# Optimization experiments

Measured on AMD Instinct MI355X. Metric: run time of the kernel, lower is better.

## Reference

```python
import jax, jax.numpy as jnp
import numpy as np

N = 100000
IN_CH, HID_CH, OUT_CH = 128, 128, 64
E = 1600000


def gcn_layer(x, W, b, src, dst, num_nodes):
    """PyG GCNConv: add self-loops, symmetric deg^-1/2 normalization,
    x' = D^-1/2 (A+I) D^-1/2 (x W) + b."""
    # degrees including self-loops (deg = 1 + in-degree with unit edge weights)
    ones = jnp.ones(dst.shape[0], dtype=x.dtype)
    deg = jnp.ones(num_nodes, dtype=x.dtype).at[dst].add(ones)
    dinv = jax.lax.rsqrt(deg)
    h = x @ W  # [N, out_dim] -- transform before propagate (PyG order)
    # neighbor messages
    norm = dinv[src] * dinv[dst]                      # [E]
    msg = h[src] * norm[:, None]                      # [E, out_dim] (traffic-bound)
    agg = jax.ops.segment_sum(msg, dst, num_segments=num_nodes)
    # self-loop contribution: norm_ii = dinv[i]^2
    agg = agg + h * (dinv * dinv)[:, None]
    return agg + b


def setup_inputs() -> dict:
    key = jax.random.key(0)
    ks = jax.random.split(key, 7)
    x = jax.random.normal(ks[0], (N, IN_CH), dtype=jnp.float32)
    edge_index = jax.random.randint(ks[1], (2, E), 0, N, dtype=jnp.int64)
    # Glorot-style init like PyG GCNConv
    W1 = jax.random.normal(ks[2], (IN_CH, HID_CH), dtype=jnp.float32) * (1.0 / np.sqrt(IN_CH))
    b1 = jnp.zeros((HID_CH,), dtype=jnp.float32)
    W2 = jax.random.normal(ks[3], (HID_CH, OUT_CH), dtype=jnp.float32) * (1.0 / np.sqrt(HID_CH))
    b2 = jnp.zeros((OUT_CH,), dtype=jnp.float32)
    return {"x": x, "edge_index": edge_index, "W1": W1, "b1": b1, "W2": W2, "b2": b2}


def reference(x, edge_index, W1, b1, W2, b2):
    src, dst = edge_index[0], edge_index[1]
    h = gcn_layer(x, W1, b1, src, dst, N)
    h = jax.nn.relu(h)  # dropout is identity in eval mode
    out = gcn_layer(h, W2, b2, src, dst, N)
    return out
```

## Files before the change

### kernel.cpp

```cpp
#include <hip/hip_runtime.h>
#include <hip/hip_fp16.h>

#define NNODES 100000
#define NEDGES 1600000
#define IN_C   128
#define HID_C  128
#define OUT_C  64

#define CAP     64
#define OVF_MAX 4096

#define BUCKET_SHIFT 7
#define BUCKET_NODES 128
#define NB ((NNODES + BUCKET_NODES - 1) / BUCKET_NODES)
#define BCAP 3072
#define EB 4096
#define NBLK_A ((NEDGES + EB - 1) / EB)

typedef __attribute__((ext_vector_type(8))) _Float16 half8;
typedef __attribute__((ext_vector_type(4))) _Float16 half4;
typedef __attribute__((ext_vector_type(4))) float floatx4;

__device__ __forceinline__ long long load_idx(const void* p, long long i, int is64) {
  return is64 ? ((const long long*)p)[i] : (long long)((const int*)p)[i];
}

__global__ void detect_idx_kernel(const void* eidx, int* flag) {
  const unsigned* w = (const unsigned*)eidx;
  int lane = threadIdx.x & 63;
  unsigned v = w[2 * lane + 1];
  unsigned long long bad = __ballot(v != 0u);
  if (lane == 0) *flag = (bad == 0ull) ? 1 : 0;
}


__global__ void zero_misc_kernel(int* bcnt, int* ovf_cnt, int* ovfA_cnt) {
  int i = blockIdx.x * 256 + threadIdx.x;
  if (i < NB) bcnt[i] = 0;
  if (i == 0) { *ovf_cnt = 0; *ovfA_cnt = 0; }
}

__global__ __launch_bounds__(256) void binA_kernel(const void* __restrict__ eidx,
                                                   const int* __restrict__ flag,
                                                   int* __restrict__ bcnt,
                                                   unsigned* __restrict__ buf,
                                                   int* __restrict__ ovfA_cnt,
                                                   int2* __restrict__ ovfA) {
  __shared__ int hist[NB];
  __shared__ int base[NB];
  __shared__ int ofs[NB];
  const int tid = threadIdx.x;
  const int e0 = blockIdx.x * EB;
  const int e1 = min(e0 + EB, NEDGES);
  const int is64 = *flag;

  for (int b = tid; b < NB; b += 256) { hist[b] = 0; ofs[b] = 0; }
  __syncthreads();

  for (int e = e0 + tid; e < e1; e += 256) {
    int d = (int)load_idx(eidx, (long long)NEDGES + e, is64);
    atomicAdd(&hist[d >> BUCKET_SHIFT], 1);
  }
  __syncthreads();

  for (int b = tid; b < NB; b += 256) {
    int h = hist[b];
    if (h > 0) base[b] = atomicAdd(&bcnt[b], h);
  }
  __syncthreads();

  for (int e = e0 + tid; e < e1; e += 256) {
    int s = (int)load_idx(eidx, e, is64);
    int d = (int)load_idx(eidx, (long long)NEDGES + e, is64);
    int b = d >> BUCKET_SHIFT;
    int ko = atomicAdd(&ofs[b], 1);
    int slot = base[b] + ko;
    if (slot < BCAP) {
      buf[(size_t)b * BCAP + slot] =
          (unsigned)s | ((unsigned)(d & (BUCKET_NODES - 1)) << 17);
    } else {
      int p = atomicAdd(ovfA_cnt, 1);
      if (p < OVF_MAX) ovfA[p] = make_int2(s, d);
    }
  }
}

__global__ __launch_bounds__(256) void binB_kernel(const int* __restrict__ bcnt,
                                                   const unsigned* __restrict__ buf,
                                                   int* __restrict__ cnt,
                                                   float* __restrict__ dinv,
                                                   int* __restrict__ pad_csr,
                                                   int* __restrict__ ovf_cnt,
                                                   int2* __restrict__ ovf) {
  __shared__ int pad[BUCKET_NODES * CAP];
  __shared__ int lcnt[BUCKET_NODES];
  const int b = blockIdx.x;
  const int tid = threadIdx.x;
  const int node0 = b << BUCKET_SHIFT;

  if (tid < BUCKET_NODES) lcnt[tid] = 0;
  __syncthreads();

  const int n = min(bcnt[b], BCAP);
  for (int k = tid; k < n; k += 256) {
    unsigned u = buf[(size_t)b * BCAP + k];
    int s = (int)(u & 0x1FFFFu);
    int dl = (int)(u >> 17);
    int slot = atomicAdd(&lcnt[dl], 1);
    if (slot < CAP) {
      pad[dl * CAP + slot] = s;
    } else {
      int p = atomicAdd(ovf_cnt, 1);
      if (p < OVF_MAX) ovf[p] = make_int2(s, node0 + dl);
    }
  }
  __syncthreads();

  constexpr int I4PN = CAP / 4;
  for (int q = tid; q < BUCKET_NODES * I4PN; q += 256) {
    int dl = q / I4PN;
    int gn = node0 + dl;
    if (gn < NNODES) {
      int c = (q % I4PN) * 4;
      *(int4*)&pad_csr[(size_t)gn * CAP + c] = *(const int4*)&pad[dl * CAP + c];
    }
  }
  if (tid < BUCKET_NODES && node0 + tid < NNODES) {
    int c = lcnt[tid];
    cnt[node0 + tid] = c;
    dinv[node0 + tid] = rsqrtf((float)(c + 1));
  }
}

__global__ void fixup_kernel(const int* __restrict__ ovfA_cnt,
                             const int2* __restrict__ ovfA,
                             int* __restrict__ cnt, float* __restrict__ dinv,
                             int* __restrict__ pad_csr,
                             int* __restrict__ ovf_cnt, int2* __restrict__ ovf) {
  int n = min(*ovfA_cnt, OVF_MAX);
  for (int t = threadIdx.x; t < n; t += 256) {
    int2 p = ovfA[t];
    int k = atomicAdd(&cnt[p.y], 1);
    if (k < CAP) {
      pad_csr[(size_t)p.y * CAP + k] = p.x;
    } else {
      int q = atomicAdd(ovf_cnt, 1);
      if (q < OVF_MAX) ovf[q] = p;
    }
  }
  __syncthreads();
  for (int t = threadIdx.x; t < n; t += 256) {
    int node = ovfA[t].y;
    dinv[node] = rsqrtf((float)(cnt[node] + 1));
  }
}

struct F8 {
  float x0, x1, x2, x3, x4, x5, x6, x7;
};

__device__ __forceinline__ void add_h8(F8& a, const __half* p) {
  int4 r = *(const int4*)p;
  const __half2* h = (const __half2*)&r;
  float2 f0 = __half22float2(h[0]);
  float2 f1 = __half22float2(h[1]);
  float2 f2 = __half22float2(h[2]);
  float2 f3 = __half22float2(h[3]);
  a.x0 += f0.x; a.x1 += f0.y; a.x2 += f1.x; a.x3 += f1.y;
  a.x4 += f2.x; a.x5 += f2.y; a.x6 += f3.x; a.x7 += f3.y;
}

template <int C, bool RELU, bool OUT16>
__global__ __launch_bounds__(256) void gather_kernel(const int* __restrict__ cnt,
                                                     const int* __restrict__ pad_csr,
                                                     const float* __restrict__ dinv,
                                                     const __half* __restrict__ Hs,
                                                     const float* __restrict__ bias,
                                                     const int* __restrict__ ovf_cnt,
                                                     const int2* __restrict__ ovf,
                                                     void* __restrict__ OutPtr) {
  constexpr int TPN = C / 8;
  int gid = blockIdx.x * 256 + threadIdx.x;
  int i = gid / TPN;
  int c8 = (gid % TPN) * 8;
  if (i >= NNODES) return;

  const float di = dinv[i];
  const int deg = cnt[i];
  const int beg = i * CAP;
  const int end = beg + min(deg, CAP);
  const int* __restrict__ lst = pad_csr;

  F8 a0 = {}, a1 = {}, a2 = {}, a3 = {};
  add_h8(a0, &Hs[(size_t)i * C + c8]);

  int j = beg;
  for (; j + 8 <= end; j += 8) {
    int4 sa = *(const int4*)&lst[j];
    int4 sb = *(const int4*)&lst[j + 4];
    add_h8(a0, &Hs[(size_t)sa.x * C + c8]);
    add_h8(a1, &Hs[(size_t)sa.y * C + c8]);
    add_h8(a2, &Hs[(size_t)sa.z * C + c8]);
    add_h8(a3, &Hs[(size_t)sa.w * C + c8]);
    add_h8(a0, &Hs[(size_t)sb.x * C + c8]);
    add_h8(a1, &Hs[(size_t)sb.y * C + c8]);
    add_h8(a2, &Hs[(size_t)sb.z * C + c8]);
    add_h8(a3, &Hs[(size_t)sb.w * C + c8]);
  }
  for (; j + 2 <= end; j += 2) {
    int s0 = lst[j + 0], s1 = lst[j + 1];
    add_h8(a0, &Hs[(size_t)s0 * C + c8]);
    add_h8(a1, &Hs[(size_t)s1 * C + c8]);
  }
  if (j < end) {
    add_h8(a0, &Hs[(size_t)lst[j] * C + c8]);
  }

  if (deg > CAP) {
    int n = min(*ovf_cnt, OVF_MAX);
    for (int t = 0; t < n; ++t) {
      int2 p = ovf[t];
      if (p.y == i) add_h8(a0, &Hs[(size_t)p.x * C + c8]);
    }
  }

  float s0 = a0.x0 + a1.x0 + a2.x0 + a3.x0;
  float s1 = a0.x1 + a1.x1 + a2.x1 + a3.x1;
  float s2 = a0.x2 + a1.x2 + a2.x2 + a3.x2;
  float s3 = a0.x3 + a1.x3 + a2.x3 + a3.x3;
  float s4 = a0.x4 + a1.x4 + a2.x4 + a3.x4;
  float s5 = a0.x5 + a1.x5 + a2.x5 + a3.x5;
  float s6 = a0.x6 + a1.x6 + a2.x6 + a3.x6;
  float s7 = a0.x7 + a1.x7 + a2.x7 + a3.x7;

  float4 b0 = *(const float4*)&bias[c8];
  float4 b1 = *(const float4*)&bias[c8 + 4];
  float o0 = fmaf(s0, di, b0.x);
  float o1 = fmaf(s1, di, b0.y);
  float o2 = fmaf(s2, di, b0.z);
  float o3 = fmaf(s3, di, b0.w);
  float o4 = fmaf(s4, di, b1.x);
  float o5 = fmaf(s5, di, b1.y);
  float o6 = fmaf(s6, di, b1.z);
  float o7 = fmaf(s7, di, b1.w);
  if (RELU) {
    o0 = o0 > 0.f ? o0 : 0.f;
    o1 = o1 > 0.f ? o1 : 0.f;
    o2 = o2 > 0.f ? o2 : 0.f;
    o3 = o3 > 0.f ? o3 : 0.f;
    o4 = o4 > 0.f ? o4 : 0.f;
    o5 = o5 > 0.f ? o5 : 0.f;
    o6 = o6 > 0.f ? o6 : 0.f;
    o7 = o7 > 0.f ? o7 : 0.f;
  }
  if (OUT16) {
    half8 hv = {(_Float16)o0, (_Float16)o1, (_Float16)o2, (_Float16)o3,
                (_Float16)o4, (_Float16)o5, (_Float16)o6, (_Float16)o7};
    *(half8*)((_Float16*)OutPtr + (size_t)i * C + c8) = hv;
  } else {
    float* Out = (float*)OutPtr;
    float4 v0 = make_float4(o0, o1, o2, o3);
    float4 v1 = make_float4(o4, o5, o6, o7);
    *(float4*)&Out[(size_t)i * C + c8] = v0;
    *(float4*)&Out[(size_t)i * C + c8 + 4] = v1;
  }
}

template <int K, int N, bool A_F16>
__global__ __launch_bounds__(256) void mfma_gemm_kernel(const void* __restrict__ Xv,
                                                        const float* __restrict__ Wm,
                                                        const float* __restrict__ scale,
                                                        _Float16* __restrict__ Hout,
                                                        int M) {
  constexpr int KP = K + 8;
  __shared__ alignas(16) _Float16 Alds[64 * KP];
  __shared__ alignas(16) _Float16 Wlds[N * KP];

  const int tid = threadIdx.x;
  const int row0 = blockIdx.x * 64;

  constexpr int TILES = (K / 4) * (N / 4);
  for (int tile = tid; tile < TILES; tile += 256) {
    int kt = tile / (N / 4);
    int nt = tile % (N / 4);
    const float* wp = &Wm[(4 * kt) * N + 4 * nt];
    float4 r0 = *(const float4*)(wp);
    float4 r1 = *(const float4*)(wp + N);
    float4 r2 = *(const float4*)(wp + 2 * N);
    float4 r3 = *(const float4*)(wp + 3 * N);
    half4 c0 = {(_Float16)r0.x, (_Float16)r1.x, (_Float16)r2.x, (_Float16)r3.x};
    half4 c1 = {(_Float16)r0.y, (_Float16)r1.y, (_Float16)r2.y, (_Float16)r3.y};
    half4 c2 = {(_Float16)r0.z, (_Float16)r1.z, (_Float16)r2.z, (_Float16)r3.z};
    half4 c3 = {(_Float16)r0.w, (_Float16)r1.w, (_Float16)r2.w, (_Float16)r3.w};
    *(half4*)&Wlds[(4 * nt + 0) * KP + 4 * kt] = c0;
    *(half4*)&Wlds[(4 * nt + 1) * KP + 4 * kt] = c1;
    *(half4*)&Wlds[(4 * nt + 2) * KP + 4 * kt] = c2;
    *(half4*)&Wlds[(4 * nt + 3) * KP + 4 * kt] = c3;
  }

  if (A_F16) {
    const _Float16* Xh = (const _Float16*)Xv;
    constexpr int H8PR = K / 8;
    constexpr int TOT = 64 * H8PR;
    for (int idx = tid; idx < TOT; idx += 256) {
      int lr = idx / H8PR;
      int c8 = (idx % H8PR) * 8;
      int gr = row0 + lr;
      if (gr > M - 1) gr = M - 1;
      int4 v = *(const int4*)&Xh[(size_t)gr * K + c8];
      *(int4*)&Alds[lr * KP + c8] = v;
    }
  } else {
    const float* Xf = (const float*)Xv;
    constexpr int F4PR = K / 4;
    constexpr int TOT = 64 * F4PR;
    for (int idx = tid; idx < TOT; idx += 256) {
      int lr = idx / F4PR;
      int c4 = (idx % F4PR) * 4;
      int gr = row0 + lr;
      if (gr > M - 1) gr = M - 1;
      float4 v = *(const float4*)&Xf[(size_t)gr * K + c4];
      half4 h = {(_Float16)v.x, (_Float16)v.y, (_Float16)v.z, (_Float16)v.w};
      *(half4*)&Alds[lr * KP + c4] = h;
    }
  }
  __syncthreads();

  const int w = tid >> 6;
  const int lane = tid & 63;
  const int g = lane >> 4;
  const int mi = lane & 15;
  constexpr int NT = N / 16;

  floatx4 acc[NT];
#pragma unroll
  for (int t = 0; t < NT; ++t) acc[t] = (floatx4){0.f, 0.f, 0.f, 0.f};

  const _Float16* arow = &Alds[(w * 16 + mi) * KP];
#pragma unroll
  for (int ks = 0; ks < K / 32; ++ks) {
    half8 a = *(const half8*)(arow + ks * 32 + g * 8);
#pragma unroll
    for (int t = 0; t < NT; ++t) {
      half8 b = *(const half8*)&Wlds[(t * 16 + mi) * KP + ks * 32 + g * 8];
      acc[t] = __builtin_amdgcn_mfma_f32_16x16x32_f16(a, b, acc[t], 0, 0, 0);
    }
  }

#pragma unroll
  for (int r = 0; r < 4; ++r) {
    int grow = row0 + w * 16 + 4 * g + r;
    if (grow < M) {
      float s = scale[grow];
      _Float16* orow = Hout + (size_t)grow * N + mi;
#pragma unroll
      for (int t = 0; t < NT; ++t) orow[t * 16] = (_Float16)(acc[t][r] * s);
    }
  }
}

extern "C" void kernel_launch(void* const* d_in, const int* in_sizes, int n_in,
                              void* d_out, int out_size, void* d_ws, size_t ws_size,
                              hipStream_t stream) {
  const float* x = (const float*)d_in[0];
  const void* eidx = d_in[1];
  const float* W1 = (const float*)d_in[2];
  const float* b1 = (const float*)d_in[3];
  const float* W2 = (const float*)d_in[4];
  const float* b2 = (const float*)d_in[5];
  float* out = (float*)d_out;
  char* ws = (char*)d_ws;

  int*      flag     = (int*)(ws + 0);
  int*      ovf_cnt  = (int*)(ws + 512);
  int*      ovfA_cnt = (int*)(ws + 1024);
  int*      bcnt     = (int*)(ws + 1536);
  int*      cnt      = (int*)(ws + 8192);
  float*    dinv     = (float*)(ws + 408576);
  int2*     ovf      = (int2*)(ws + 809472);
  int2*     ovfA     = (int2*)(ws + 842752);
  unsigned* buf      = (unsigned*)(ws + 876032);
  int*      pad_csr  = (int*)(ws + 10486272);
  _Float16* h1       = (_Float16*)(ws + 36086784);
  _Float16* hidden   = (_Float16*)(ws + 61687296);
  _Float16* h2 = h1;

  detect_idx_kernel<<<1, 64, 0, stream>>>(eidx, flag);
  zero_misc_kernel<<<(NB + 255) / 256, 256, 0, stream>>>(bcnt, ovf_cnt, ovfA_cnt);
  binA_kernel<<<NBLK_A, 256, 0, stream>>>(eidx, flag, bcnt, buf, ovfA_cnt, ovfA);
  binB_kernel<<<NB, 256, 0, stream>>>(bcnt, buf, cnt, dinv, pad_csr, ovf_cnt, ovf);
  fixup_kernel<<<1, 256, 0, stream>>>(ovfA_cnt, ovfA, cnt, dinv, pad_csr,
                                      ovf_cnt, ovf);

  const int GB = (NNODES + 63) / 64;

  mfma_gemm_kernel<IN_C, HID_C, false>
      <<<GB, 256, 0, stream>>>(x, W1, dinv, h1, NNODES);
  gather_kernel<HID_C, true, true>
      <<<(NNODES * (HID_C / 8) + 255) / 256, 256, 0, stream>>>(cnt, pad_csr, dinv,
                                                               (const __half*)h1, b1,
                                                               ovf_cnt, ovf, hidden);
  mfma_gemm_kernel<HID_C, OUT_C, true>
      <<<GB, 256, 0, stream>>>(hidden, W2, dinv, h2, NNODES);
  gather_kernel<OUT_C, false, false>
      <<<(NNODES * (OUT_C / 8) + 255) / 256, 256, 0, stream>>>(cnt, pad_csr, dinv,
                                                               (const __half*)h2, b2,
                                                               ovf_cnt, ovf, out);
}
```

Baseline: 281.4 us.

## Cache edges in LDS during binning, pad bucket counters, widen gather to 16 channels

The binning pass now reads each edge once into shared memory and reuses it for the scatter phase instead of re-reading the edge list from global memory. Global bucket counters are padded to separate cache lines, and each block visits buckets in a rotated order to reduce atomic contention. The gather kernel has each thread handle 16 channels with two accumulator pairs instead of 8 channels with four, halving index loads per node but lowering thread count and ILP per load stream. The workspace offsets shift to make room for the padded counters.

Result: no change. 277.0 us (-1.6%).

```diff
diff --git a/kernel.cpp b/kernel.cpp
--- a/kernel.cpp
+++ b/kernel.cpp
@@ -14,6 +14,7 @@
 #define BUCKET_NODES 128
 #define NB ((NNODES + BUCKET_NODES - 1) / BUCKET_NODES)
 #define BCAP 3072
+#define BCNT_STRIDE 16
 #define EB 4096
 #define NBLK_A ((NEDGES + EB - 1) / EB)
 
@@ -36,7 +37,7 @@
 
 __global__ void zero_misc_kernel(int* bcnt, int* ovf_cnt, int* ovfA_cnt) {
   int i = blockIdx.x * 256 + threadIdx.x;
-  if (i < NB) bcnt[i] = 0;
+  if (i < NB * BCNT_STRIDE) bcnt[i] = 0;
   if (i == 0) { *ovf_cnt = 0; *ovfA_cnt = 0; }
 }
 
@@ -46,41 +47,52 @@
                                                    unsigned* __restrict__ buf,
                                                    int* __restrict__ ovfA_cnt,
                                                    int2* __restrict__ ovfA) {
+  __shared__ unsigned se[EB];
+  __shared__ unsigned short be[EB];
   __shared__ int hist[NB];
   __shared__ int base[NB];
   __shared__ int ofs[NB];
   const int tid = threadIdx.x;
   const int e0 = blockIdx.x * EB;
   const int e1 = min(e0 + EB, NEDGES);
+  const int m = e1 - e0;
   const int is64 = *flag;
 
   for (int b = tid; b < NB; b += 256) { hist[b] = 0; ofs[b] = 0; }
   __syncthreads();
 
-  for (int e = e0 + tid; e < e1; e += 256) {
-    int d = (int)load_idx(eidx, (long long)NEDGES + e, is64);
-    atomicAdd(&hist[d >> BUCKET_SHIFT], 1);
-  }
-  __syncthreads();
-
-  for (int b = tid; b < NB; b += 256) {
-    int h = hist[b];
-    if (h > 0) base[b] = atomicAdd(&bcnt[b], h);
-  }
-  __syncthreads();
-
-  for (int e = e0 + tid; e < e1; e += 256) {
+  for (int k = tid; k < m; k += 256) {
+    int e = e0 + k;
     int s = (int)load_idx(eidx, e, is64);
     int d = (int)load_idx(eidx, (long long)NEDGES + e, is64);
     int b = d >> BUCKET_SHIFT;
+    se[k] = (unsigned)s | ((unsigned)(d & (BUCKET_NODES - 1)) << 17);
+    be[k] = (unsigned short)b;
+    atomicAdd(&hist[b], 1);
+  }
+  __syncthreads();
+
+  int rot = (blockIdx.x * 131) % NB;
+  for (int idx = tid; idx < NB; idx += 256) {
+    int b = idx + rot;
+    if (b >= NB) b -= NB;
+    int h = hist[b];
+    if (h > 0) base[b] = atomicAdd(&bcnt[b * BCNT_STRIDE], h);
+  }
+  __syncthreads();
+
+  for (int k = tid; k < m; k += 256) {
+    unsigned u = se[k];
+    int b = be[k];
     int ko = atomicAdd(&ofs[b], 1);
     int slot = base[b] + ko;
     if (slot < BCAP) {
-      buf[(size_t)b * BCAP + slot] =
-          (unsigned)s | ((unsigned)(d & (BUCKET_NODES - 1)) << 17);
+      buf[(size_t)b * BCAP + slot] = u;
     } else {
       int p = atomicAdd(ovfA_cnt, 1);
-      if (p < OVF_MAX) ovfA[p] = make_int2(s, d);
+      if (p < OVF_MAX)
+        ovfA[p] = make_int2((int)(u & 0x1FFFFu),
+                            (b << BUCKET_SHIFT) | (int)(u >> 17));
     }
   }
 }
@@ -101,7 +113,7 @@
   if (tid < BUCKET_NODES) lcnt[tid] = 0;
   __syncthreads();
 
-  const int n = min(bcnt[b], BCAP);
+  const int n = min(bcnt[b * BCNT_STRIDE], BCAP);
   for (int k = tid; k < n; k += 256) {
     unsigned u = buf[(size_t)b * BCAP + k];
     int s = (int)(u & 0x1FFFFu);
@@ -179,10 +191,10 @@
                                                      const int* __restrict__ ovf_cnt,
                                                      const int2* __restrict__ ovf,
                                                      void* __restrict__ OutPtr) {
-  constexpr int TPN = C / 8;
+  constexpr int TPN = C / 16;
   int gid = blockIdx.x * 256 + threadIdx.x;
   int i = gid / TPN;
-  int c8 = (gid % TPN) * 8;
+  int c16 = (gid % TPN) * 16;
   if (i >= NNODES) return;
 
   const float di = dinv[i];
@@ -190,79 +202,103 @@
   const int beg = i * CAP;
   const int end = beg + min(deg, CAP);
   const int* __restrict__ lst = pad_csr;
-
-  F8 a0 = {}, a1 = {}, a2 = {}, a3 = {};
-  add_h8(a0, &Hs[(size_t)i * C + c8]);
+  const __half* __restrict__ Hb = Hs + c16;
+
+  F8 a0l = {}, a0h = {}, a1l = {}, a1h = {};
+  {
+    const __half* p = Hb + (size_t)i * C;
+    add_h8(a0l, p);
+    add_h8(a0h, p + 8);
+  }
 
   int j = beg;
   for (; j + 8 <= end; j += 8) {
     int4 sa = *(const int4*)&lst[j];
     int4 sb = *(const int4*)&lst[j + 4];
-    add_h8(a0, &Hs[(size_t)sa.x * C + c8]);
-    add_h8(a1, &Hs[(size_t)sa.y * C + c8]);
-    add_h8(a2, &Hs[(size_t)sa.z * C + c8]);
-    add_h8(a3, &Hs[(size_t)sa.w * C + c8]);
-    add_h8(a0, &Hs[(size_t)sb.x * C + c8]);
-    add_h8(a1, &Hs[(size_t)sb.y * C + c8]);
-    add_h8(a2, &Hs[(size_t)sb.z * C + c8]);
-    add_h8(a3, &Hs[(size_t)sb.w * C + c8]);
+    const __half* p0 = Hb + (size_t)sa.x * C;
+    const __half* p1 = Hb + (size_t)sa.y * C;
+    const __half* p2 = Hb + (size_t)sa.z * C;
+    const __half* p3 = Hb + (size_t)sa.w * C;
+    add_h8(a0l, p0); add_h8(a0h, p0 + 8);
+    add_h8(a1l, p1); add_h8(a1h, p1 + 8);
+    add_h8(a0l, p2); add_h8(a0h, p2 + 8);
+    add_h8(a1l, p3); add_h8(a1h, p3 + 8);
+    const __half* p4 = Hb + (size_t)sb.x * C;
+    const __half* p5 = Hb + (size_t)sb.y * C;
+    const __half* p6 = Hb + (size_t)sb.z * C;
+    const __half* p7 = Hb + (size_t)sb.w * C;
+    add_h8(a0l, p4); add_h8(a0h, p4 + 8);
+    add_h8(a1l, p5); add_h8(a1h, p5 + 8);
+    add_h8(a0l, p6); add_h8(a0h, p6 + 8);
+    add_h8(a1l, p7); add_h8(a1h, p7 + 8);
   }
   for (; j + 2 <= end; j += 2) {
-    int s0 = lst[j + 0], s1 = lst[j + 1];
-    add_h8(a0, &Hs[(size_t)s0 * C + c8]);
-    add_h8(a1, &Hs[(size_t)s1 * C + c8]);
+    const __half* p0 = Hb + (size_t)lst[j] * C;
+    const __half* p1 = Hb + (size_t)lst[j + 1] * C;
+    add_h8(a0l, p0); add_h8(a0h, p0 + 8);
+    add_h8(a1l, p1); add_h8(a1h, p1 + 8);
   }
   if (j < end) {
-    add_h8(a0, &Hs[(size_t)lst[j] * C + c8]);
+    const __half* p0 = Hb + (size_t)lst[j] * C;
+    add_h8(a0l, p0); add_h8(a0h, p0 + 8);
   }
 
   if (deg > CAP) {
     int n = min(*ovf_cnt, OVF_MAX);
     for (int t = 0; t < n; ++t) {
       int2 p = ovf[t];
-      if (p.y == i) add_h8(a0, &Hs[(size_t)p.x * C + c8]);
-    }
-  }
-
-  float s0 = a0.x0 + a1.x0 + a2.x0 + a3.x0;
-  float s1 = a0.x1 + a1.x1 + a2.x1 + a3.x1;
-  float s2 = a0.x2 + a1.x2 + a2.x2 + a3.x2;
-  float s3 = a0.x3 + a1.x3 + a2.x3 + a3.x3;
-  float s4 = a0.x4 + a1.x4 + a2.x4 + a3.x4;
-  float s5 = a0.x5 + a1.x5 + a2.x5 + a3.x5;
-  float s6 = a0.x6 + a1.x6 + a2.x6 + a3.x6;
-  float s7 = a0.x7 + a1.x7 + a2.x7 + a3.x7;
-
-  float4 b0 = *(const float4*)&bias[c8];
-  float4 b1 = *(const float4*)&bias[c8 + 4];
-  float o0 = fmaf(s0, di, b0.x);
-  float o1 = fmaf(s1, di, b0.y);
-  float o2 = fmaf(s2, di, b0.z);
-  float o3 = fmaf(s3, di, b0.w);
-  float o4 = fmaf(s4, di, b1.x);
-  float o5 = fmaf(s5, di, b1.y);
-  float o6 = fmaf(s6, di, b1.z);
-  float o7 = fmaf(s7, di, b1.w);
+      if (p.y == i) {
+        const __half* q = Hb + (size_t)p.x * C;
+        add_h8(a0l, q); add_h8(a0h, q + 8);
+      }
+    }
+  }
+
+  float s0 = a0l.x0 + a1l.x0, s1 = a0l.x1 + a1l.x1;
+  float s2 = a0l.x2 + a1l.x2, s3 = a0l.x3 + a1l.x3;
+  float s4 = a0l.x4 + a1l.x4, s5 = a0l.x5 + a1l.x5;
+  float s6 = a0l.x6 + a1l.x6, s7 = a0l.x7 + a1l.x7;
+  float s8 = a0h.x0 + a1h.x0, s9 = a0h.x1 + a1h.x1;
+  float s10 = a0h.x2 + a1h.x2, s11 = a0h.x3 + a1h.x3;
+  float s12 = a0h.x4 + a1h.x4, s13 = a0h.x5 + a1h.x5;
+  float s14 = a0h.x6 + a1h.x6, s15 = a0h.x7 + a1h.x7;
+
+  float4 b0 = *(const float4*)&bias[c16];
+  float4 b1 = *(const float4*)&bias[c16 + 4];
+  float4 b2 = *(const float4*)&bias[c16 + 8];
+  float4 b3 = *(const float4*)&bias[c16 + 12];
+  float o0 = fmaf(s0, di, b0.x),  o1 = fmaf(s1, di, b0.y);
+  float o2 = fmaf(s2, di, b0.z),  o3 = fmaf(s3, di, b0.w);
+  float o4 = fmaf(s4, di, b1.x),  o5 = fmaf(s5, di, b1.y);
+  float o6 = fmaf(s6, di, b1.z),  o7 = fmaf(s7, di, b1.w);
+  float o8 = fmaf(s8, di, b2.x),  o9 = fmaf(s9, di, b2.y);
+  float o10 = fmaf(s10, di, b2.z), o11 = fmaf(s11, di, b2.w);
+  float o12 = fmaf(s12, di, b3.x), o13 = fmaf(s13, di, b3.y);
+  float o14 = fmaf(s14, di, b3.z), o15 = fmaf(s15, di, b3.w);
   if (RELU) {
-    o0 = o0 > 0.f ? o0 : 0.f;
-    o1 = o1 > 0.f ? o1 : 0.f;
-    o2 = o2 > 0.f ? o2 : 0.f;
-    o3 = o3 > 0.f ? o3 : 0.f;
-    o4 = o4 > 0.f ? o4 : 0.f;
-    o5 = o5 > 0.f ? o5 : 0.f;
-    o6 = o6 > 0.f ? o6 : 0.f;
-    o7 = o7 > 0.f ? o7 : 0.f;
+    o0 = o0 > 0.f ? o0 : 0.f;   o1 = o1 > 0.f ? o1 : 0.f;
+    o2 = o2 > 0.f ? o2 : 0.f;   o3 = o3 > 0.f ? o3 : 0.f;
+    o4 = o4 > 0.f ? o4 : 0.f;   o5 = o5 > 0.f ? o5 : 0.f;
+    o6 = o6 > 0.f ? o6 : 0.f;   o7 = o7 > 0.f ? o7 : 0.f;
+    o8 = o8 > 0.f ? o8 : 0.f;   o9 = o9 > 0.f ? o9 : 0.f;
+    o10 = o10 > 0.f ? o10 : 0.f; o11 = o11 > 0.f ? o11 : 0.f;
+    o12 = o12 > 0.f ? o12 : 0.f; o13 = o13 > 0.f ? o13 : 0.f;
+    o14 = o14 > 0.f ? o14 : 0.f; o15 = o15 > 0.f ? o15 : 0.f;
   }
   if (OUT16) {
-    half8 hv = {(_Float16)o0, (_Float16)o1, (_Float16)o2, (_Float16)o3,
-                (_Float16)o4, (_Float16)o5, (_Float16)o6, (_Float16)o7};
-    *(half8*)((_Float16*)OutPtr + (size_t)i * C + c8) = hv;
+    _Float16* Out = (_Float16*)OutPtr + (size_t)i * C + c16;
+    half8 hv0 = {(_Float16)o0, (_Float16)o1, (_Float16)o2, (_Float16)o3,
+                 (_Float16)o4, (_Float16)o5, (_Float16)o6, (_Float16)o7};
+    half8 hv1 = {(_Float16)o8, (_Float16)o9, (_Float16)o10, (_Float16)o11,
+                 (_Float16)o12, (_Float16)o13, (_Float16)o14, (_Float16)o15};
+    *(half8*)Out = hv0;
+    *(half8*)(Out + 8) = hv1;
   } else {
-    float* Out = (float*)OutPtr;
-    float4 v0 = make_float4(o0, o1, o2, o3);
-    float4 v1 = make_float4(o4, o5, o6, o7);
-    *(float4*)&Out[(size_t)i * C + c8] = v0;
-    *(float4*)&Out[(size_t)i * C + c8 + 4] = v1;
+    float* Out = (float*)OutPtr + (size_t)i * C + c16;
+    *(float4*)Out = make_float4(o0, o1, o2, o3);
+    *(float4*)(Out + 4) = make_float4(o4, o5, o6, o7);
+    *(float4*)(Out + 8) = make_float4(o8, o9, o10, o11);
+    *(float4*)(Out + 12) = make_float4(o12, o13, o14, o15);
   }
 }
 
@@ -375,35 +411,35 @@
   int*      ovf_cnt  = (int*)(ws + 512);
   int*      ovfA_cnt = (int*)(ws + 1024);
   int*      bcnt     = (int*)(ws + 1536);
-  int*      cnt      = (int*)(ws + 8192);
-  float*    dinv     = (float*)(ws + 408576);
-  int2*     ovf      = (int2*)(ws + 809472);
-  int2*     ovfA     = (int2*)(ws + 842752);
-  unsigned* buf      = (unsigned*)(ws + 876032);
-  int*      pad_csr  = (int*)(ws + 10486272);
-  _Float16* h1       = (_Float16*)(ws + 36086784);
-  _Float16* hidden   = (_Float16*)(ws + 61687296);
+  int*      cnt      = (int*)(ws + 52224);
+  float*    dinv     = (float*)(ws + 452608);
+  int2*     ovf      = (int2*)(ws + 852992);
+  int2*     ovfA     = (int2*)(ws + 885760);
+  unsigned* buf      = (unsigned*)(ws + 918528);
+  int*      pad_csr  = (int*)(ws + 10528256);
+  _Float16* h1       = (_Float16*)(ws + 36128256);
+  _Float16* hidden   = (_Float16*)(ws + 61728256);
   _Float16* h2 = h1;
 
   detect_idx_kernel<<<1, 64, 0, stream>>>(eidx, flag);
-  zero_misc_kernel<<<(NB + 255) / 256, 256, 0, stream>>>(bcnt, ovf_cnt, ovfA_cnt);
+  zero_misc_kernel<<<(NB * BCNT_STRIDE + 255) / 256, 256, 0, stream>>>(bcnt, ovf_cnt,
+                                                                       ovfA_cnt);
   binA_kernel<<<NBLK_A, 256, 0, stream>>>(eidx, flag, bcnt, buf, ovfA_cnt, ovfA);
   binB_kernel<<<NB, 256, 0, stream>>>(bcnt, buf, cnt, dinv, pad_csr, ovf_cnt, ovf);
   fixup_kernel<<<1, 256, 0, stream>>>(ovfA_cnt, ovfA, cnt, dinv, pad_csr,
                                       ovf_cnt, ovf);
 
   const int GB = (NNODES + 63) / 64;
-
   mfma_gemm_kernel<IN_C, HID_C, false>
       <<<GB, 256, 0, stream>>>(x, W1, dinv, h1, NNODES);
   gather_kernel<HID_C, true, true>
-      <<<(NNODES * (HID_C / 8) + 255) / 256, 256, 0, stream>>>(cnt, pad_csr, dinv,
-                                                               (const __half*)h1, b1,
-                                                               ovf_cnt, ovf, hidden);
+      <<<(NNODES * (HID_C / 16) + 255) / 256, 256, 0, stream>>>(cnt, pad_csr, dinv,
+                                                                (const __half*)h1, b1,
+                                                                ovf_cnt, ovf, hidden);
   mfma_gemm_kernel<HID_C, OUT_C, true>
       <<<GB, 256, 0, stream>>>(hidden, W2, dinv, h2, NNODES);
   gather_kernel<OUT_C, false, false>
-      <<<(NNODES * (OUT_C / 8) + 255) / 256, 256, 0, stream>>>(cnt, pad_csr, dinv,
-                                                               (const __half*)h2, b2,
-                                                               ovf_cnt, ovf, out);
-}
+      <<<(NNODES * (OUT_C / 16) + 255) / 256, 256, 0, stream>>>(cnt, pad_csr, dinv,
+                                                                (const __half*)h2, b2,
+                                                                ovf_cnt, ovf, out);
+}
```
